# Kernel optimization log

Hardware: AMD Instinct MI355X
Metric: run time of the kernel (lower is better)

## Reference

```python
import jax, jax.numpy as jnp
import numpy as np


def setup_inputs() -> dict:
    key = jax.random.key(0)
    ks = jax.random.split(key, 8)
    B, S, Ta, D = 64, 512, 8, 768
    return {
        "memory": jax.random.normal(ks[0], (B, S, D), dtype=jnp.float32),
        "aspect_states": jax.random.normal(ks[1], (B, Ta, D), dtype=jnp.float32),
        "input_ids": jnp.ones((B, S), dtype=jnp.int64),
        "input_t_ids": jnp.ones((B, Ta), dtype=jnp.int64),
        "W1": jax.random.normal(ks[2], (3 * D, D), dtype=jnp.float32) * 0.02,
        "b1": jnp.zeros((D,), dtype=jnp.float32),
        "w2": jax.random.normal(ks[3], (D,), dtype=jnp.float32) * 0.02,
        "Wm": jax.random.normal(ks[4], (D, D), dtype=jnp.float32) * 0.02,
        "bm": jnp.zeros((D,), dtype=jnp.float32),
        "Wd": jax.random.normal(ks[5], (D, 3), dtype=jnp.float32) * 0.02,
        "bd": jnp.zeros((3,), dtype=jnp.float32),
    }


def reference(memory, aspect_states, input_ids, input_t_ids, W1, b1, w2, Wm, bm, Wd, bd):
    B, S, D = memory.shape
    memory_len = jnp.sum(input_ids != 0, axis=-1)          # [B]
    aspect_len = jnp.sum(input_t_ids != 0, axis=-1)        # [B]

    # v_a: mean-pooled aspect representation  [B, D]
    v_a = jnp.sum(aspect_states, axis=1) / aspect_len.astype(memory.dtype)[:, None]
    # v_s: mean-pooled sentence representation [B, D]
    v_s = jnp.sum(memory, axis=1) / memory_len.astype(memory.dtype)[:, None]

    # locationed_memory: memory[i, idx] *= 1 - idx/memory_len[i] for idx < memory_len[i]
    idx = jnp.arange(S, dtype=memory.dtype)                 # [S]
    mlen = memory_len.astype(memory.dtype)[:, None]         # [B, 1]
    loc = jnp.where(idx[None, :] < mlen, 1.0 - idx[None, :] / mlen, 1.0)  # [B, S]
    memory = memory * loc[:, :, None]

    # chunked linear1/linear2 scorer, vectorized:
    # c_t = w2 . tanh(W1 @ [m_t ; v_a ; v_s] + b1)
    W1_m, W1_a, W1_s = W1[:D], W1[D:2 * D], W1[2 * D:]
    ctx = v_a @ W1_a + v_s @ W1_s + b1                      # [B, D]
    h = jnp.tanh(jnp.einsum("bsd,de->bse", memory, W1_m) + ctx[:, None, :])
    scores = h @ w2                                         # [B, S]
    alpha = jax.nn.softmax(scores, axis=1)

    v_ts = jnp.einsum("bsd,bs->bd", memory, alpha)          # [B, D]
    v_ns = v_ts + v_s
    v_ms = jnp.tanh(v_ns @ Wm + bm)
    logits = v_ms @ Wd + bd                                 # [B, 3]
    return logits
```

## Files before the change

### kernel.cpp

```cpp
#include <hip/hip_runtime.h>
#include <hip/hip_bf16.h>


#define NB 64
#define NS 512
#define ND 768
#define NTA 8

typedef __attribute__((ext_vector_type(8))) __bf16 bf16x8;
typedef __attribute__((ext_vector_type(4))) float f32x4;

#define OFF_PVS 0u
#define OFF_PVTS 6291456u
#define OFF_PCTX 9437184u
#define OFF_CTX 10223616u
#define OFF_PU 10420224u
#define OFF_PSC 11206656u
#define OFF_ALPHA 12779520u
#define OFF_VS 12910592u
#define OFF_VA 13107200u
#define OFF_LENS 13303808u
#define OFF_W1MT 13304832u
#define OFF_MP 14484480u

__device__ __forceinline__ float fast_tanh(float x) {
  x = fminf(fmaxf(x, -15.f), 15.f);
  float t = __expf(2.f * x);
  return __fdividef(t - 1.f, t + 1.f);
}

__device__ __forceinline__ unsigned bfpack2(float a, float b) {
  unsigned ua = __float_as_uint(a), ub = __float_as_uint(b);
  ua = (ua + 0x7FFFu + ((ua >> 16) & 1u)) >> 16;
  ub = (ub + 0x7FFFu + ((ub >> 16) & 1u)) >> 16;
  return ua | (ub << 16);
}

__device__ __forceinline__ unsigned short bf16b(float f) {
  unsigned u = __float_as_uint(f);
  u = (u + 0x7FFFu + ((u >> 16) & 1u)) >> 16;
  return (unsigned short)u;
}

__device__ __forceinline__ void async_copy16(const void* g, void* l) {
  __builtin_amdgcn_global_load_lds(
      (const __attribute__((address_space(1))) void*)g,
      (__attribute__((address_space(3))) void*)l, 16, 0, 0);
}

__global__ __launch_bounds__(256) void k_prep_tr(const int* __restrict__ ids,
                                                 const int* __restrict__ tids,
                                                 const float* __restrict__ aspect,
                                                 const float* __restrict__ W1,
                                                 float* __restrict__ v_a,
                                                 float* __restrict__ lens,
                                                 unsigned short* __restrict__ w1mt) {
  int bid = blockIdx.x, tid = threadIdx.x;
  if (bid < 576) {
    __shared__ float tile[32][33];
    int bx = bid % 24, by = bid / 24;
    int tx = tid & 31, ty = tid >> 5;
    for (int j = 0; j < 32; j += 8)
      tile[ty + j][tx] = W1[(size_t)(by * 32 + ty + j) * ND + bx * 32 + tx];
    __syncthreads();
    for (int j = 0; j < 32; j += 8)
      w1mt[(size_t)(bx * 32 + ty + j) * ND + by * 32 + tx] = bf16b(tile[tx][ty + j]);
  } else {
    int b = bid - 576;
    __shared__ int red[256];
    __shared__ float sh_inva;
    int cnt = 0;
    for (int j = tid; j < NS; j += 256) cnt += (ids[b * NS + j] != 0);
    red[tid] = cnt;
    __syncthreads();
    for (int s = 128; s > 0; s >>= 1) {
      if (tid < s) red[tid] += red[tid + s];
      __syncthreads();
    }
    if (tid == 0) {
      int mlen = red[0];
      int acnt = 0;
      for (int t = 0; t < NTA; ++t) acnt += (tids[b * NTA + t] != 0);
      lens[b] = (float)mlen;
      lens[64 + b] = 1.0f / (float)mlen;
      float inva = 1.0f / (float)acnt;
      lens[128 + b] = inva;
      sh_inva = inva;
    }
    __syncthreads();
    float inva = sh_inva;
    for (int j = tid; j < ND; j += 256) {
      float s = 0.f;
      for (int t = 0; t < NTA; ++t) s += aspect[((size_t)b * NTA + t) * ND + j];
      v_a[b * ND + j] = s * inva;
    }
  }
}

__global__ __launch_bounds__(192) void k_vs_mprime(const float* __restrict__ memory,
                                                   const float* __restrict__ lens,
                                                   float* __restrict__ part_vs,
                                                   unsigned short* __restrict__ mp) {
  int sc = blockIdx.x, b = blockIdx.y, tid = threadIdx.x;
  int d0 = tid * 4;
  float inv_mlen = lens[64 + b];
  float mlenf = lens[b];
  float s0 = 0, s1 = 0, s2 = 0, s3 = 0;
#pragma unroll
  for (int s = 0; s < 16; ++s) {
    int srow = sc * 16 + s;
    size_t row = (size_t)b * NS + srow;
    const float4 v = *(const float4*)(memory + row * ND + d0);
    s0 += v.x; s1 += v.y; s2 += v.z; s3 += v.w;
    float fs = (float)srow;
    float loc = (fs < mlenf) ? 1.0f - fs * inv_mlen : 1.0f;
    uint2 pk;
    pk.x = bfpack2(v.x * loc, v.y * loc);
    pk.y = bfpack2(v.z * loc, v.w * loc);
    *(uint2*)(mp + row * ND + d0) = pk;
  }
  float4 o;
  o.x = s0 * inv_mlen; o.y = s1 * inv_mlen; o.z = s2 * inv_mlen; o.w = s3 * inv_mlen;
  *(float4*)(part_vs + ((size_t)sc * NB + b) * ND + d0) = o;
}

__global__ __launch_bounds__(192) void k_reduce_vs(const float* __restrict__ part_vs,
                                                   float* __restrict__ v_s) {
  int b = blockIdx.x, tid = threadIdx.x;
  int d0 = tid * 4;
  float a0 = 0, a1 = 0, a2 = 0, a3 = 0;
#pragma unroll
  for (int p = 0; p < 32; ++p) {
    const float4 v = *(const float4*)(part_vs + ((size_t)p * NB + b) * ND + d0);
    a0 += v.x; a1 += v.y; a2 += v.z; a3 += v.w;
  }
  float4 o; o.x = a0; o.y = a1; o.z = a2; o.w = a3;
  *(float4*)(v_s + b * ND + d0) = o;
}

__global__ __launch_bounds__(128) void k_ctx(const float* __restrict__ W1,
                                             const float* __restrict__ v_a,
                                             const float* __restrict__ v_s,
                                             float* __restrict__ ctx_part) {
  int b = blockIdx.x, et = blockIdx.y, dc = blockIdx.z, tid = threadIdx.x;
  __shared__ float vbuf[384];
  for (int j = tid; j < 384; j += 128) {
    int k = dc * 384 + j;
    vbuf[j] = (k < ND) ? v_a[b * ND + k] : v_s[b * ND + (k - ND)];
  }
  __syncthreads();
  int e = et * 128 + tid;
  float acc = 0.f;
  const float* Wk = W1 + (size_t)(ND + dc * 384) * ND + e;
#pragma unroll 8
  for (int j = 0; j < 384; ++j) acc += vbuf[j] * Wk[(size_t)j * ND];
  ctx_part[((size_t)dc * NB + b) * ND + e] = acc;
}

__global__ __launch_bounds__(192) void k_reduce_ctx(const float* __restrict__ ctx_part,
                                                    const float* __restrict__ b1,
                                                    float* __restrict__ ctx) {
  int b = blockIdx.x, tid = threadIdx.x;
  int d0 = tid * 4;
  const float4 bb = *(const float4*)(b1 + d0);
  float a0 = bb.x, a1 = bb.y, a2 = bb.z, a3 = bb.w;
#pragma unroll
  for (int p = 0; p < 4; ++p) {
    const float4 v = *(const float4*)(ctx_part + ((size_t)p * NB + b) * ND + d0);
    a0 += v.x; a1 += v.y; a2 += v.z; a3 += v.w;
  }
  float4 o; o.x = a0; o.y = a1; o.z = a2; o.w = a3;
  *(float4*)(ctx + b * ND + d0) = o;
}

__global__ __launch_bounds__(256) void k_gemm_scores(const unsigned short* __restrict__ mp,
                                                     const unsigned short* __restrict__ w1mt,
                                                     const float* __restrict__ ctx,
                                                     const float* __restrict__ w2,
                                                     float* __restrict__ sc_part) {
  __shared__ char lds[65536];
  const int tid = threadIdx.x;
  const int wave = tid >> 6, lane = tid & 63;
  const int bid = blockIdx.x;
  const int swz = (bid & 7) * 192 + (bid >> 3);
  const int rt = swz / 6;
  const int et = swz - rt * 6;
  const int row0 = rt * 128, n0 = et * 128;
  const int b = row0 >> 9;
  const int wm = wave & 1, wn = wave >> 1;

  const int lrow = lane >> 3;
  const int qlog = (lane & 7) ^ lrow;
  const char* Abase = (const char*)mp + (size_t)(row0 + lrow) * (ND * 2) + qlog * 16;
  const char* Bbase = (const char*)w1mt + (size_t)(n0 + lrow) * (ND * 2) + qlog * 16;

  f32x4 acc[4][4];
#pragma unroll
  for (int i = 0; i < 4; ++i)
#pragma unroll
    for (int t = 0; t < 4; ++t) acc[i][t] = (f32x4){0.f, 0.f, 0.f, 0.f};

  const int q2 = lane >> 4, c = lane & 15;
  int offA[4][2], offB[4][2];
#pragma unroll
  for (int i = 0; i < 4; ++i) {
    int ml = wm * 64 + i * 16 + c;
    offA[i][0] = ml * 128 + ((q2 ^ (ml & 7)) * 16);
    offA[i][1] = ml * 128 + (((4 + q2) ^ (ml & 7)) * 16);
    int nl = wn * 64 + i * 16 + c;
    offB[i][0] = nl * 128 + ((q2 ^ (nl & 7)) * 16);
    offB[i][1] = nl * 128 + (((4 + q2) ^ (nl & 7)) * 16);
  }

  auto stage = [&](int bufsel, int kb) {
    char* lA = lds + bufsel * 32768;
    char* lB = lA + 16384;
#pragma unroll
    for (int i = 0; i < 4; ++i) {
      int g = wave * 4 + i;
      async_copy16(Abase + (size_t)g * 8 * (ND * 2) + kb, lA + g * 1024);
      async_copy16(Bbase + (size_t)g * 8 * (ND * 2) + kb, lB + g * 1024);
    }
  };

  stage(0, 0);
  __syncthreads();

  int cur = 0;
#pragma unroll 2
  for (int t = 0; t < 12; ++t) {
    if (t < 11) stage(cur ^ 1, (t + 1) * 128);
    const char* lA = lds + cur * 32768;
    const char* lB = lA + 16384;
    bf16x8 af[2][4], bfr[2][4];
#pragma unroll
    for (int kk = 0; kk < 2; ++kk)
#pragma unroll
      for (int i = 0; i < 4; ++i) {
        af[kk][i] = *(const bf16x8*)(lA + offA[i][kk]);
        bfr[kk][i] = *(const bf16x8*)(lB + offB[i][kk]);
      }
#pragma unroll
    for (int kk = 0; kk < 2; ++kk)
#pragma unroll
      for (int i = 0; i < 4; ++i)
#pragma unroll
        for (int t2 = 0; t2 < 4; ++t2)
          acc[i][t2] = __builtin_amdgcn_mfma_f32_16x16x32_bf16(af[kk][i], bfr[kk][t2], acc[i][t2], 0, 0, 0);
    __syncthreads();
    cur ^= 1;
  }

  float ctxv[4], w2v[4];
#pragma unroll
  for (int t = 0; t < 4; ++t) {
    int n = n0 + wn * 64 + t * 16 + c;
    ctxv[t] = ctx[b * ND + n];
    w2v[t] = w2[n];
  }
  float* scp = sc_part + (size_t)(et * 2 + wn) * (NB * NS);
#pragma unroll
  for (int i = 0; i < 4; ++i) {
#pragma unroll
    for (int r = 0; r < 4; ++r) {
      float s = 0.f;
#pragma unroll
      for (int t = 0; t < 4; ++t) s += fast_tanh(acc[i][t][r] + ctxv[t]) * w2v[t];
      s += __shfl_xor(s, 1, 64);
      s += __shfl_xor(s, 2, 64);
      s += __shfl_xor(s, 4, 64);
      s += __shfl_xor(s, 8, 64);
      if (c == 0) scp[row0 + wm * 64 + i * 16 + q2 * 4 + r] = s;
    }
  }
}

__global__ __launch_bounds__(512) void k_softmax(const float* __restrict__ sc_part,
                                                 float* __restrict__ alpha) {
  int b = blockIdx.x, tid = threadIdx.x;
  int wid = tid >> 6, lane = tid & 63;
  __shared__ float red[8], red2[8];
  float v = 0.f;
#pragma unroll
  for (int p = 0; p < 12; ++p) v += sc_part[(size_t)p * (NB * NS) + b * NS + tid];
  float m = v;
  for (int off = 1; off < 64; off <<= 1) m = fmaxf(m, __shfl_xor(m, off, 64));
  if (lane == 0) red[wid] = m;
  __syncthreads();
  if (tid == 0) {
    float mm = red[0];
    for (int i = 1; i < 8; ++i) mm = fmaxf(mm, red[i]);
    red[0] = mm;
  }
  __syncthreads();
  float M = red[0];
  float e = __expf(v - M);
  float s = e;
  for (int off = 1; off < 64; off <<= 1) s += __shfl_xor(s, off, 64);
  if (lane == 0) red2[wid] = s;
  __syncthreads();
  if (tid == 0) {
    float ss = 0.f;
    for (int i = 0; i < 8; ++i) ss += red2[i];
    red2[0] = ss;
  }
  __syncthreads();
  alpha[b * NS + tid] = e / red2[0];
}

__global__ __launch_bounds__(192) void k_vts(const unsigned short* __restrict__ mp,
                                             const float* __restrict__ alpha,
                                             float* __restrict__ part_vts) {
  int sc = blockIdx.x, b = blockIdx.y, tid = threadIdx.x;
  __shared__ float al[32];
  if (tid < 32) al[tid] = alpha[b * NS + sc * 32 + tid];
  __syncthreads();
  int d0 = tid * 4;
  float a0 = 0, a1 = 0, a2 = 0, a3 = 0;
#pragma unroll 8
  for (int s = 0; s < 32; ++s) {
    size_t row = (size_t)b * NS + sc * 32 + s;
    uint2 pk = *(const uint2*)(mp + row * ND + d0);
    float a = al[s];
    a0 += a * __uint_as_float(pk.x << 16);
    a1 += a * __uint_as_float(pk.x & 0xFFFF0000u);
    a2 += a * __uint_as_float(pk.y << 16);
    a3 += a * __uint_as_float(pk.y & 0xFFFF0000u);
  }
  float4 o; o.x = a0; o.y = a1; o.z = a2; o.w = a3;
  *(float4*)(part_vts + ((size_t)sc * NB + b) * ND + d0) = o;
}

__global__ __launch_bounds__(128) void k_final1(const float* __restrict__ part_vts,
                                                const float* __restrict__ v_s,
                                                const float* __restrict__ Wm,
                                                float* __restrict__ u_part) {
  int b = blockIdx.x, et = blockIdx.y, dc = blockIdx.z, tid = threadIdx.x;
  __shared__ float vbuf[192];
  for (int j = tid; j < 192; j += 128) {
    int d = dc * 192 + j;
    float v = v_s[b * ND + d];
#pragma unroll
    for (int p = 0; p < 16; ++p) v += part_vts[((size_t)p * NB + b) * ND + d];
    vbuf[j] = v;
  }
  __syncthreads();
  int e = et * 128 + tid;
  float acc = 0.f;
  const float* Wk = Wm + (size_t)(dc * 192) * ND + e;
#pragma unroll 8
  for (int j = 0; j < 192; ++j) acc += vbuf[j] * Wk[(size_t)j * ND];
  u_part[((size_t)dc * NB + b) * ND + e] = acc;
}

__global__ __launch_bounds__(256) void k_final2(const float* __restrict__ u_part,
                                                const float* __restrict__ bm,
                                                const float* __restrict__ Wd,
                                                const float* __restrict__ bd,
                                                float* __restrict__ out) {
  int b = blockIdx.x, tid = threadIdx.x;
  int wid = tid >> 6, lane = tid & 63;
  __shared__ float red[4][3];
  float p0 = 0, p1 = 0, p2 = 0;
  for (int e = tid; e < ND; e += 256) {
    float uv = bm[e];
#pragma unroll
    for (int dc = 0; dc < 4; ++dc) uv += u_part[((size_t)dc * NB + b) * ND + e];
    float vm = fast_tanh(uv);
    p0 += vm * Wd[e * 3 + 0];
    p1 += vm * Wd[e * 3 + 1];
    p2 += vm * Wd[e * 3 + 2];
  }
  for (int off = 1; off < 64; off <<= 1) {
    p0 += __shfl_xor(p0, off, 64);
    p1 += __shfl_xor(p1, off, 64);
    p2 += __shfl_xor(p2, off, 64);
  }
  if (lane == 0) { red[wid][0] = p0; red[wid][1] = p1; red[wid][2] = p2; }
  __syncthreads();
  if (tid == 0) {
    out[b * 3 + 0] = red[0][0] + red[1][0] + red[2][0] + red[3][0] + bd[0];
    out[b * 3 + 1] = red[0][1] + red[1][1] + red[2][1] + red[3][1] + bd[1];
    out[b * 3 + 2] = red[0][2] + red[1][2] + red[2][2] + red[3][2] + bd[2];
  }
}

extern "C" void kernel_launch(void* const* d_in, const int* in_sizes, int n_in,
                              void* d_out, int out_size, void* d_ws, size_t ws_size,
                              hipStream_t stream) {
  const float* memory = (const float*)d_in[0];
  const float* aspect = (const float*)d_in[1];
  const int* ids = (const int*)d_in[2];
  const int* tids = (const int*)d_in[3];
  const float* W1 = (const float*)d_in[4];
  const float* b1 = (const float*)d_in[5];
  const float* w2 = (const float*)d_in[6];
  const float* Wm = (const float*)d_in[7];
  const float* bm = (const float*)d_in[8];
  const float* Wd = (const float*)d_in[9];
  const float* bd = (const float*)d_in[10];
  float* out = (float*)d_out;

  char* ws = (char*)d_ws;
  float* part_vs = (float*)(ws + OFF_PVS);
  float* part_vts = (float*)(ws + OFF_PVTS);
  float* ctx_part = (float*)(ws + OFF_PCTX);
  float* ctx = (float*)(ws + OFF_CTX);
  float* u_part = (float*)(ws + OFF_PU);
  float* sc_part = (float*)(ws + OFF_PSC);
  float* alpha = (float*)(ws + OFF_ALPHA);
  float* v_s = (float*)(ws + OFF_VS);
  float* v_a = (float*)(ws + OFF_VA);
  float* lens = (float*)(ws + OFF_LENS);
  unsigned short* w1mt = (unsigned short*)(ws + OFF_W1MT);
  unsigned short* mp = (unsigned short*)(ws + OFF_MP);


  k_prep_tr<<<640, 256, 0, stream>>>(ids, tids, aspect, W1, v_a, lens, w1mt);
  k_vs_mprime<<<dim3(32, NB), 192, 0, stream>>>(memory, lens, part_vs, mp);
  k_reduce_vs<<<NB, 192, 0, stream>>>(part_vs, v_s);
  k_ctx<<<dim3(64, 6, 4), 128, 0, stream>>>(W1, v_a, v_s, ctx_part);
  k_reduce_ctx<<<NB, 192, 0, stream>>>(ctx_part, b1, ctx);
  k_gemm_scores<<<1536, 256, 0, stream>>>(mp, w1mt, ctx, w2, sc_part);
  k_softmax<<<NB, 512, 0, stream>>>(sc_part, alpha);
  k_vts<<<dim3(16, NB), 192, 0, stream>>>(mp, alpha, part_vts);
  k_final1<<<dim3(64, 6, 4), 128, 0, stream>>>(part_vts, v_s, Wm, u_part);
  k_final2<<<NB, 256, 0, stream>>>(u_part, bm, Wd, bd, out);
}
```

Measured before the change: 303.3 us.

## Enlarge scores GEMM tile to 256x128 with triple-buffered async LDS pipeline

Doubles the M tile of the fused scores GEMM to 256 rows with 8 waves per block, halving the grid so each W1 tile staged in LDS is reused across more rows. Replaces the double buffer with a three-slot LDS ring that prefetches two k-steps ahead, using explicit vmcnt waits and bare s_barrier instead of __syncthreads. It also raises wave priority around the MFMA block. The 144 KB of LDS allows only one block per CU and the hand-counted waits are fragile if the number of outstanding copies changes.

```diff
diff --git a/kernel.cpp b/kernel.cpp
--- a/kernel.cpp
+++ b/kernel.cpp
@@ -173,21 +173,21 @@
   *(float4*)(ctx + b * ND + d0) = o;
 }
 
-__global__ __launch_bounds__(256) void k_gemm_scores(const unsigned short* __restrict__ mp,
+__global__ __launch_bounds__(512) void k_gemm_scores(const unsigned short* __restrict__ mp,
                                                      const unsigned short* __restrict__ w1mt,
                                                      const float* __restrict__ ctx,
                                                      const float* __restrict__ w2,
                                                      float* __restrict__ sc_part) {
-  __shared__ char lds[65536];
+  __shared__ char lds[147456];
   const int tid = threadIdx.x;
   const int wave = tid >> 6, lane = tid & 63;
   const int bid = blockIdx.x;
-  const int swz = (bid & 7) * 192 + (bid >> 3);
+  const int swz = (bid & 7) * 96 + (bid >> 3);
   const int rt = swz / 6;
   const int et = swz - rt * 6;
-  const int row0 = rt * 128, n0 = et * 128;
+  const int row0 = rt * 256, n0 = et * 128;
   const int b = row0 >> 9;
-  const int wm = wave & 1, wn = wave >> 1;
+  const int wm = wave & 3, wn = wave >> 2;
 
   const int lrow = lane >> 3;
   const int qlog = (lane & 7) ^ lrow;
@@ -207,39 +207,48 @@
     int ml = wm * 64 + i * 16 + c;
     offA[i][0] = ml * 128 + ((q2 ^ (ml & 7)) * 16);
     offA[i][1] = ml * 128 + (((4 + q2) ^ (ml & 7)) * 16);
-    int nl = wn * 64 + i * 16 + c;
-    offB[i][0] = nl * 128 + ((q2 ^ (nl & 7)) * 16);
-    offB[i][1] = nl * 128 + (((4 + q2) ^ (nl & 7)) * 16);
-  }
-
-  auto stage = [&](int bufsel, int kb) {
-    char* lA = lds + bufsel * 32768;
-    char* lB = lA + 16384;
+  }
+#pragma unroll
+  for (int t = 0; t < 4; ++t) {
+    int nl = wn * 64 + t * 16 + c;
+    offB[t][0] = nl * 128 + ((q2 ^ (nl & 7)) * 16);
+    offB[t][1] = nl * 128 + (((4 + q2) ^ (nl & 7)) * 16);
+  }
+
+  auto stage = [&](int slot, int kb) {
+    char* lA = lds + slot * 49152;
+    char* lB = lA + 32768;
 #pragma unroll
     for (int i = 0; i < 4; ++i) {
       int g = wave * 4 + i;
       async_copy16(Abase + (size_t)g * 8 * (ND * 2) + kb, lA + g * 1024);
+    }
+#pragma unroll
+    for (int i = 0; i < 2; ++i) {
+      int g = wave * 2 + i;
       async_copy16(Bbase + (size_t)g * 8 * (ND * 2) + kb, lB + g * 1024);
     }
   };
 
   stage(0, 0);
-  __syncthreads();
-
-  int cur = 0;
-#pragma unroll 2
-  for (int t = 0; t < 12; ++t) {
-    if (t < 11) stage(cur ^ 1, (t + 1) * 128);
-    const char* lA = lds + cur * 32768;
-    const char* lB = lA + 16384;
+  stage(1, 128);
+  asm volatile("s_waitcnt vmcnt(6)" ::: "memory");
+  __builtin_amdgcn_s_barrier();
+
+#pragma unroll
+  for (int u = 0; u < 12; ++u) {
+    if (u + 2 < 12) stage((u + 2) % 3, (u + 2) * 128);
+    const char* lA = lds + (u % 3) * 49152;
+    const char* lB = lA + 32768;
     bf16x8 af[2][4], bfr[2][4];
 #pragma unroll
-    for (int kk = 0; kk < 2; ++kk)
-#pragma unroll
-      for (int i = 0; i < 4; ++i) {
-        af[kk][i] = *(const bf16x8*)(lA + offA[i][kk]);
-        bfr[kk][i] = *(const bf16x8*)(lB + offB[i][kk]);
-      }
+    for (int kk = 0; kk < 2; ++kk) {
+#pragma unroll
+      for (int i = 0; i < 4; ++i) af[kk][i] = *(const bf16x8*)(lA + offA[i][kk]);
+#pragma unroll
+      for (int t2 = 0; t2 < 4; ++t2) bfr[kk][t2] = *(const bf16x8*)(lB + offB[t2][kk]);
+    }
+    __builtin_amdgcn_s_setprio(1);
 #pragma unroll
     for (int kk = 0; kk < 2; ++kk)
 #pragma unroll
@@ -247,8 +256,10 @@
 #pragma unroll
         for (int t2 = 0; t2 < 4; ++t2)
           acc[i][t2] = __builtin_amdgcn_mfma_f32_16x16x32_bf16(af[kk][i], bfr[kk][t2], acc[i][t2], 0, 0, 0);
-    __syncthreads();
-    cur ^= 1;
+    __builtin_amdgcn_s_setprio(0);
+    if (u < 10)      { asm volatile("s_waitcnt vmcnt(6)" ::: "memory"); }
+    else if (u == 10){ asm volatile("s_waitcnt vmcnt(0)" ::: "memory"); }
+    if (u < 11) __builtin_amdgcn_s_barrier();
   }
 
   float ctxv[4], w2v[4];
@@ -421,7 +432,7 @@
   k_reduce_vs<<<NB, 192, 0, stream>>>(part_vs, v_s);
   k_ctx<<<dim3(64, 6, 4), 128, 0, stream>>>(W1, v_a, v_s, ctx_part);
   k_reduce_ctx<<<NB, 192, 0, stream>>>(ctx_part, b1, ctx);
-  k_gemm_scores<<<1536, 256, 0, stream>>>(mp, w1mt, ctx, w2, sc_part);
+  k_gemm_scores<<<768, 512, 0, stream>>>(mp, w1mt, ctx, w2, sc_part);
   k_softmax<<<NB, 512, 0, stream>>>(sc_part, alpha);
   k_vts<<<dim3(16, NB), 192, 0, stream>>>(mp, alpha, part_vts);
   k_final1<<<dim3(64, 6, 4), 128, 0, stream>>>(part_vts, v_s, Wm, u_part);
```

Measured after the change: 301.2 us (median of 2 runs). No clear change (-0.7%).
